# Kernel optimization log

Hardware: AMD Instinct MI355X
Metric: run time of the kernel (lower is better)

## Reference

```python
import jax, jax.numpy as jnp
import numpy as np

NUM_HEADS = 16
HEAD_DIM = 64
BSZ, SEQ, EMBED = 2, 2048, NUM_HEADS * HEAD_DIM
SCALE = HEAD_DIM ** (-0.5)
NEG = -1e9  # large negative for masked positions (finite, fp16-unsafe values avoided)


def setup_inputs() -> dict:
    key = jax.random.key(0)
    kq, kk, kv = jax.random.split(key, 3)
    q = jax.random.normal(kq, (BSZ, SEQ, EMBED), dtype=jnp.float32)
    k = jax.random.normal(kk, (BSZ, SEQ, EMBED), dtype=jnp.float32)
    v = jax.random.normal(kv, (BSZ, SEQ, EMBED), dtype=jnp.float32)
    # additive causal mask: 0 on/below diagonal, NEG above, shape (bsz,1,tgt,src)
    causal = jnp.where(jnp.tril(jnp.ones((SEQ, SEQ), dtype=bool)), 0.0, NEG).astype(jnp.float32)
    causal = jnp.broadcast_to(causal[None, None], (BSZ, 1, SEQ, SEQ))
    return {"query_states": q, "key_states": k, "value_states": v,
            "causal_attention_mask": causal}


def reference(query_states, key_states, value_states, causal_attention_mask):
    bsz, tgt_len, embed_dim = query_states.shape
    # [b, h, s, d]
    def shape_heads(t):
        return t.reshape(bsz, -1, NUM_HEADS, HEAD_DIM).transpose(0, 2, 1, 3)
    q = shape_heads(query_states * SCALE)
    k = shape_heads(key_states)
    v = shape_heads(value_states)
    # scores: [b, h, tgt, src]
    attn_weights = jnp.einsum('bhqd,bhkd->bhqk', q, k)
    attn_weights = attn_weights + causal_attention_mask  # broadcast over heads
    attn_probs = jax.nn.softmax(attn_weights, axis=-1)
    # dropout p=0.0 / eval mode -> identity
    attn_output = jnp.einsum('bhqk,bhkd->bhqd', attn_probs, v)
    attn_output = attn_output.transpose(0, 2, 1, 3).reshape(bsz, tgt_len, embed_dim)
    return attn_output
```

## Files before the change

kernel.cpp:

```cpp
#include <hip/hip_runtime.h>
#include <hip/hip_bf16.h>
#include <stdint.h>

#define BSZ 2
#define SEQ 2048
#define NHEADS 16
#define HDIM 64
#define EMBED (NHEADS * HDIM)
#define NQT 32

#define QSCALE 0.1803368801111244f
#define C2 11.5416914f

typedef unsigned short u16;
typedef unsigned int u32;
typedef __attribute__((ext_vector_type(8))) short bf16x8;
typedef __attribute__((ext_vector_type(4))) float f32x4;

#define TILE_B 8192
#define WSV_BYTE_OFF (32ull * 32 * TILE_B)

__device__ __forceinline__ u32 pkbf(float x, float y) {
  union { __hip_bfloat162 h; u32 u; } c;
  c.h = __float22bfloat162_rn(make_float2(x, y));
  return c.u;
}

__device__ __forceinline__ void gload16(const void* g, void* l) {
  __builtin_amdgcn_global_load_lds(
      (const __attribute__((address_space(1))) u32*)g,
      (__attribute__((address_space(3))) u32*)l, 16, 0, 0);
}

__global__ __launch_bounds__(256) void prep_k(const float* __restrict__ K,
                                              char* __restrict__ wsK) {
  const int t = blockIdx.x * 256 + threadIdx.x;
  const int c0 = (t & 7) * 8;
  const int h = (t >> 3) & 15;
  const size_t bs = (size_t)(t >> 7);
  const int s = (int)(bs & 2047);
  const int b = (int)(bs >> 11);
  const float* p = K + bs * EMBED + h * HDIM + c0;
  const float4 a = *reinterpret_cast<const float4*>(p);
  const float4 d = *reinterpret_cast<const float4*>(p + 4);
  uint4 out;
  out.x = pkbf(a.x, a.y); out.y = pkbf(a.z, a.w);
  out.z = pkbf(d.x, d.y); out.w = pkbf(d.z, d.w);
  const int kap = s & 63, kt = s >> 6;
  const int rho = (kap & 3) * 16 + (kap >> 2);
  char* dst = wsK + (((size_t)(b * 16 + h)) * 32 + kt) * TILE_B + rho * 128 +
              ((2 * c0) ^ ((rho & 7) << 4));
  *reinterpret_cast<uint4*>(dst) = out;
}

__global__ __launch_bounds__(256) void prep_v(const float* __restrict__ V,
                                              char* __restrict__ wsV) {
  __shared__ float tile[64][68];
  const int blk = blockIdx.x;
  const int kt = blk & 31, bh = blk >> 5;
  const int b = bh >> 4, h = bh & 15;
  const float* src = V + ((size_t)b * SEQ + kt * 64) * EMBED + h * HDIM;
  const int t = threadIdx.x;
  {
    const int row = t >> 2, c0 = (t & 3) * 16;
    const float* p = src + (size_t)row * EMBED + c0;
#pragma unroll
    for (int j = 0; j < 4; ++j)
      *reinterpret_cast<float4*>(&tile[row][c0 + 4 * j]) =
          *reinterpret_cast<const float4*>(p + 4 * j);
  }
  __syncthreads();
  const int d = t & 63, w = t >> 6;
  char* dst = wsV + ((size_t)bh * 32 + kt) * TILE_B + d * 128;
#pragma unroll
  for (int half = 0; half < 2; ++half) {
    const int kv0 = w * 8 + half * 32;
    uint4 out;
    out.x = pkbf(tile[kv0 + 0][d], tile[kv0 + 1][d]);
    out.y = pkbf(tile[kv0 + 2][d], tile[kv0 + 3][d]);
    out.z = pkbf(tile[kv0 + 4][d], tile[kv0 + 5][d]);
    out.w = pkbf(tile[kv0 + 6][d], tile[kv0 + 7][d]);
    *reinterpret_cast<uint4*>(dst + ((2 * kv0) ^ ((d & 7) << 4))) = out;
  }
}

__global__ __launch_bounds__(256, 3) void mha_fwd(const float* __restrict__ Q,
                                                  const char* __restrict__ wsK,
                                                  const char* __restrict__ wsV,
                                                  float* __restrict__ O) {
  __shared__ char Kl[2][TILE_B];
  __shared__ char Vl[2][TILE_B];
  __shared__ u16 Ps[64][72];

  const int id = ((blockIdx.x & 7) << 6) | (blockIdx.x >> 3);
  const int qlo = id & 15, bh = id >> 4;
  const int qhi = (NQT - 1) - qlo;
  const int b = bh >> 4, h = bh & 15;

  const int wave = threadIdx.x >> 6;
  const int lane = threadIdx.x & 63;
  const int fr = lane & 15;
  const int hi4 = lane >> 4;
  const int fk = hi4 * 8;
  const int crow = hi4 * 4;
  const int swz = (fr & 7) << 4;
  const int cOff0 = (hi4 * 16) ^ swz;
  const int cOff1 = cOff0 ^ 64;

  const float* qrow = Q + ((size_t)b * SEQ + wave * 16 + fr) * EMBED + h * HDIM;
  bf16x8 qlo0, qlo1, qhi0, qhi1;
  {
    union { uint4 u; bf16x8 v; } cv;
    const float* plo = qrow + (size_t)qlo * 64 * EMBED;
    const float* phi = qrow + (size_t)qhi * 64 * EMBED;
#define LOADQ(dst, base, col)                                              \
    {                                                                      \
      const float4 a = *reinterpret_cast<const float4*>((base) + (col));   \
      const float4 d = *reinterpret_cast<const float4*>((base) + (col)+4); \
      cv.u.x = pkbf(a.x * QSCALE, a.y * QSCALE);                           \
      cv.u.y = pkbf(a.z * QSCALE, a.w * QSCALE);                           \
      cv.u.z = pkbf(d.x * QSCALE, d.y * QSCALE);                           \
      cv.u.w = pkbf(d.z * QSCALE, d.w * QSCALE);                           \
      dst = cv.v;                                                          \
    }
    LOADQ(qlo0, plo, fk) LOADQ(qlo1, plo, 32 + fk)
    LOADQ(qhi0, phi, fk) LOADQ(qhi1, phi, 32 + fk)
#undef LOADQ
  }

  const char* gK = wsK + (size_t)bh * 32 * TILE_B;
  const char* gV = wsV + (size_t)bh * 32 * TILE_B;
  const int wo = wave * 2048;

  gload16(gK + wo + lane * 16, Kl[0] + wo);
  gload16(gK + wo + 1024 + lane * 16, Kl[0] + wo + 1024);
  gload16(gV + wo + lane * 16, Vl[0] + wo);
  gload16(gV + wo + 1024 + lane * 16, Vl[0] + wo + 1024);
  __syncthreads();

  const f32x4 fzero = {0.f, 0.f, 0.f, 0.f};
  f32x4 oacc_lo[4], oacc_hi[4];
  float l_lo[4], l_hi[4];
#pragma unroll
  for (int i = 0; i < 4; ++i) {
    oacc_lo[i] = fzero;
    oacc_hi[i] = fzero;
    l_lo[i] = 0.f;
    l_hi[i] = 0.f;
  }

  int cur = 0;
  for (int kt = 0; kt <= qhi; ++kt) {
    if (kt < qhi) {
      const char* nk = gK + (size_t)(kt + 1) * TILE_B;
      const char* nv = gV + (size_t)(kt + 1) * TILE_B;
      char* dK = Kl[cur ^ 1] + wo;
      char* dV = Vl[cur ^ 1] + wo;
      gload16(nk + wo + lane * 16, dK);
      gload16(nk + wo + 1024 + lane * 16, dK + 1024);
      gload16(nv + wo + lane * 16, dV);
      gload16(nv + wo + 1024 + lane * 16, dV + 1024);
    }

#pragma unroll
    for (int stream = 0; stream < 2; ++stream) {
      if (stream == 1 && kt > qlo) break;
      const bf16x8 qf0 = stream ? qlo0 : qhi0;
      const bf16x8 qf1 = stream ? qlo1 : qhi1;
      const bool diag = (kt == (stream ? qlo : qhi));
      f32x4* oacc = stream ? oacc_lo : oacc_hi;
      float* l_part = stream ? l_lo : l_hi;

      f32x4 s[4];
      __builtin_amdgcn_s_setprio(1);
#pragma unroll
      for (int n = 0; n < 4; ++n) {
        const char* krow = Kl[cur] + (n * 16 + fr) * 128;
        const bf16x8 kf0 = *reinterpret_cast<const bf16x8*>(krow + cOff0);
        const bf16x8 kf1 = *reinterpret_cast<const bf16x8*>(krow + cOff1);
        s[n] = fzero;
        s[n] = __builtin_amdgcn_mfma_f32_16x16x32_bf16(qf0, kf0, s[n], 0, 0, 0);
        s[n] = __builtin_amdgcn_mfma_f32_16x16x32_bf16(qf1, kf1, s[n], 0, 0, 0);
      }
      __builtin_amdgcn_s_setprio(0);

      if (diag) {
#pragma unroll
        for (int n = 0; n < 4; ++n)
#pragma unroll
          for (int r = 0; r < 4; ++r)
            if (4 * fr + n > wave * 16 + crow + r) s[n][r] = -1.0e30f;
      }

#pragma unroll
      for (int r = 0; r < 4; ++r) {
        const float e0 = __builtin_amdgcn_exp2f(s[0][r] - C2);
        const float e1 = __builtin_amdgcn_exp2f(s[1][r] - C2);
        const float e2 = __builtin_amdgcn_exp2f(s[2][r] - C2);
        const float e3 = __builtin_amdgcn_exp2f(s[3][r] - C2);
        l_part[r] += (e0 + e1) + (e2 + e3);
        uint2 pw;
        pw.x = pkbf(e0, e1);
        pw.y = pkbf(e2, e3);
        *reinterpret_cast<uint2*>(reinterpret_cast<char*>(&Ps[0][0]) +
                                  (wave * 16 + crow + r) * 144 + fr * 8) = pw;
      }

      __builtin_amdgcn_s_setprio(1);
#pragma unroll
      for (int kk = 0; kk < 2; ++kk) {
        const bf16x8 pf = *reinterpret_cast<const bf16x8*>(
            reinterpret_cast<const char*>(&Ps[0][0]) + (wave * 16 + fr) * 144 +
            kk * 64 + fk * 2);
#pragma unroll
        for (int nd = 0; nd < 4; ++nd) {
          const bf16x8 vf = *reinterpret_cast<const bf16x8*>(
              Vl[cur] + (nd * 16 + fr) * 128 + (kk ? cOff1 : cOff0));
          oacc[nd] = __builtin_amdgcn_mfma_f32_16x16x32_bf16(pf, vf, oacc[nd], 0, 0, 0);
        }
      }
      __builtin_amdgcn_s_setprio(0);
    }

    if (kt < qhi) __syncthreads();
    cur ^= 1;
  }

#pragma unroll
  for (int stream = 0; stream < 2; ++stream) {
    float* l_part = stream ? l_lo : l_hi;
    f32x4* oacc = stream ? oacc_lo : oacc_hi;
#pragma unroll
    for (int d = 1; d < 16; d <<= 1)
#pragma unroll
      for (int r = 0; r < 4; ++r)
        l_part[r] += __shfl_xor(l_part[r], d, 64);
    float inv_l[4];
#pragma unroll
    for (int r = 0; r < 4; ++r) inv_l[r] = 1.0f / l_part[r];
    const int qt = stream ? qlo : qhi;
    float* outg =
        O + ((size_t)b * SEQ + (size_t)qt * 64 + wave * 16) * EMBED + h * HDIM;
#pragma unroll
    for (int nd = 0; nd < 4; ++nd)
#pragma unroll
      for (int r = 0; r < 4; ++r)
        outg[(size_t)(crow + r) * EMBED + nd * 16 + fr] = oacc[nd][r] * inv_l[r];
  }
}

extern "C" void kernel_launch(void* const* d_in, const int* in_sizes, int n_in,
                              void* d_out, int out_size, void* d_ws, size_t ws_size,
                              hipStream_t stream) {
  const float* q = (const float*)d_in[0];
  const float* k = (const float*)d_in[1];
  const float* v = (const float*)d_in[2];
  float* o = (float*)d_out;
  char* wsK = (char*)d_ws;
  char* wsV = wsK + WSV_BYTE_OFF;

  prep_k<<<dim3(2048), dim3(256), 0, stream>>>(k, wsK);
  prep_v<<<dim3(1024), dim3(256), 0, stream>>>(v, wsV);
  mha_fwd<<<dim3(512), dim3(256), 0, stream>>>(q, wsK, wsV, o);
}
```

Baseline: 57.66 us.

## Split KV loop across two blocks per query pair and add combine pass

```diff
diff --git a/kernel.cpp b/kernel.cpp
--- a/kernel.cpp
+++ b/kernel.cpp
@@ -18,7 +18,10 @@
 typedef __attribute__((ext_vector_type(4))) float f32x4;
 
 #define TILE_B 8192
-#define WSV_BYTE_OFF (32ull * 32 * TILE_B)
+#define WSV_OFF (8ull * 1024 * 1024)
+#define WSO_OFF (16ull * 1024 * 1024)
+#define WSO_HALF_U16 (4ull * 1024 * 1024)
+#define WSL_OFF (32ull * 1024 * 1024)
 
 __device__ __forceinline__ u32 pkbf(float x, float y) {
   union { __hip_bfloat162 h; u32 u; } c;
@@ -26,74 +29,81 @@
   return c.u;
 }
 
+__device__ __forceinline__ u16 f2bf(float x) {
+  union { float f; u32 u; } v;
+  v.f = x;
+  u32 r = v.u + 0x7fffu + ((v.u >> 16) & 1u);
+  return (u16)(r >> 16);
+}
+
 __device__ __forceinline__ void gload16(const void* g, void* l) {
   __builtin_amdgcn_global_load_lds(
       (const __attribute__((address_space(1))) u32*)g,
       (__attribute__((address_space(3))) u32*)l, 16, 0, 0);
 }
 
-__global__ __launch_bounds__(256) void prep_k(const float* __restrict__ K,
-                                              char* __restrict__ wsK) {
-  const int t = blockIdx.x * 256 + threadIdx.x;
-  const int c0 = (t & 7) * 8;
-  const int h = (t >> 3) & 15;
-  const size_t bs = (size_t)(t >> 7);
-  const int s = (int)(bs & 2047);
-  const int b = (int)(bs >> 11);
-  const float* p = K + bs * EMBED + h * HDIM + c0;
-  const float4 a = *reinterpret_cast<const float4*>(p);
-  const float4 d = *reinterpret_cast<const float4*>(p + 4);
-  uint4 out;
-  out.x = pkbf(a.x, a.y); out.y = pkbf(a.z, a.w);
-  out.z = pkbf(d.x, d.y); out.w = pkbf(d.z, d.w);
-  const int kap = s & 63, kt = s >> 6;
-  const int rho = (kap & 3) * 16 + (kap >> 2);
-  char* dst = wsK + (((size_t)(b * 16 + h)) * 32 + kt) * TILE_B + rho * 128 +
-              ((2 * c0) ^ ((rho & 7) << 4));
-  *reinterpret_cast<uint4*>(dst) = out;
-}
-
-__global__ __launch_bounds__(256) void prep_v(const float* __restrict__ V,
-                                              char* __restrict__ wsV) {
+__global__ __launch_bounds__(256) void prep_kv(const float* __restrict__ K,
+                                               const float* __restrict__ V,
+                                               char* __restrict__ ws) {
   __shared__ float tile[64][68];
-  const int blk = blockIdx.x;
-  const int kt = blk & 31, bh = blk >> 5;
-  const int b = bh >> 4, h = bh & 15;
-  const float* src = V + ((size_t)b * SEQ + kt * 64) * EMBED + h * HDIM;
-  const int t = threadIdx.x;
-  {
-    const int row = t >> 2, c0 = (t & 3) * 16;
-    const float* p = src + (size_t)row * EMBED + c0;
-#pragma unroll
-    for (int j = 0; j < 4; ++j)
-      *reinterpret_cast<float4*>(&tile[row][c0 + 4 * j]) =
-          *reinterpret_cast<const float4*>(p + 4 * j);
-  }
-  __syncthreads();
-  const int d = t & 63, w = t >> 6;
-  char* dst = wsV + ((size_t)bh * 32 + kt) * TILE_B + d * 128;
-#pragma unroll
-  for (int half = 0; half < 2; ++half) {
-    const int kv0 = w * 8 + half * 32;
+  if (blockIdx.x < 2048) {
+    const int t = blockIdx.x * 256 + threadIdx.x;
+    const int c0 = (t & 7) * 8;
+    const int h = (t >> 3) & 15;
+    const size_t bs = (size_t)(t >> 7);
+    const int s = (int)(bs & 2047);
+    const int b = (int)(bs >> 11);
+    const float* p = K + bs * EMBED + h * HDIM + c0;
+    const float4 a = *reinterpret_cast<const float4*>(p);
+    const float4 d = *reinterpret_cast<const float4*>(p + 4);
     uint4 out;
-    out.x = pkbf(tile[kv0 + 0][d], tile[kv0 + 1][d]);
-    out.y = pkbf(tile[kv0 + 2][d], tile[kv0 + 3][d]);
-    out.z = pkbf(tile[kv0 + 4][d], tile[kv0 + 5][d]);
-    out.w = pkbf(tile[kv0 + 6][d], tile[kv0 + 7][d]);
-    *reinterpret_cast<uint4*>(dst + ((2 * kv0) ^ ((d & 7) << 4))) = out;
+    out.x = pkbf(a.x, a.y); out.y = pkbf(a.z, a.w);
+    out.z = pkbf(d.x, d.y); out.w = pkbf(d.z, d.w);
+    const int kap = s & 63, kt = s >> 6;
+    const int rho = (kap & 3) * 16 + (kap >> 2);
+    char* dst = ws + (((size_t)(b * 16 + h)) * 32 + kt) * TILE_B + rho * 128 +
+                ((2 * c0) ^ ((rho & 7) << 4));
+    *reinterpret_cast<uint4*>(dst) = out;
+  } else {
+    const int blk = blockIdx.x - 2048;
+    const int kt = blk & 31, bh = blk >> 5;
+    const int b = bh >> 4, h = bh & 15;
+    const float* src = V + ((size_t)b * SEQ + kt * 64) * EMBED + h * HDIM;
+    const int t = threadIdx.x;
+    {
+      const int row = t >> 2, c0 = (t & 3) * 16;
+      const float* p = src + (size_t)row * EMBED + c0;
+#pragma unroll
+      for (int j = 0; j < 4; ++j)
+        *reinterpret_cast<float4*>(&tile[row][c0 + 4 * j]) =
+            *reinterpret_cast<const float4*>(p + 4 * j);
+    }
+    __syncthreads();
+    const int d = t & 63, w = t >> 6;
+    char* dst = ws + WSV_OFF + ((size_t)bh * 32 + kt) * TILE_B + d * 128;
+#pragma unroll
+    for (int half = 0; half < 2; ++half) {
+      const int kv0 = w * 8 + half * 32;
+      uint4 out;
+      out.x = pkbf(tile[kv0 + 0][d], tile[kv0 + 1][d]);
+      out.y = pkbf(tile[kv0 + 2][d], tile[kv0 + 3][d]);
+      out.z = pkbf(tile[kv0 + 4][d], tile[kv0 + 5][d]);
+      out.w = pkbf(tile[kv0 + 6][d], tile[kv0 + 7][d]);
+      *reinterpret_cast<uint4*>(dst + ((2 * kv0) ^ ((d & 7) << 4))) = out;
+    }
   }
 }
 
 __global__ __launch_bounds__(256, 3) void mha_fwd(const float* __restrict__ Q,
-                                                  const char* __restrict__ wsK,
-                                                  const char* __restrict__ wsV,
-                                                  float* __restrict__ O) {
+                                                  char* __restrict__ ws) {
   __shared__ char Kl[2][TILE_B];
   __shared__ char Vl[2][TILE_B];
   __shared__ u16 Ps[64][72];
 
-  const int id = ((blockIdx.x & 7) << 6) | (blockIdx.x >> 3);
-  const int qlo = id & 15, bh = id >> 4;
+  const int id = ((blockIdx.x & 7) << 7) | (blockIdx.x >> 3);
+  const int half = id & 1;
+  const int qlo = (id >> 1) & 15;
+  const int bh = id >> 5;
   const int qhi = (NQT - 1) - qlo;
   const int b = bh >> 4, h = bh & 15;
 
@@ -128,14 +138,14 @@
 #undef LOADQ
   }
 
-  const char* gK = wsK + (size_t)bh * 32 * TILE_B;
-  const char* gV = wsV + (size_t)bh * 32 * TILE_B;
+  const char* gK = ws + (size_t)bh * 32 * TILE_B;
+  const char* gV = ws + WSV_OFF + (size_t)bh * 32 * TILE_B;
   const int wo = wave * 2048;
 
-  gload16(gK + wo + lane * 16, Kl[0] + wo);
-  gload16(gK + wo + 1024 + lane * 16, Kl[0] + wo + 1024);
-  gload16(gV + wo + lane * 16, Vl[0] + wo);
-  gload16(gV + wo + 1024 + lane * 16, Vl[0] + wo + 1024);
+  gload16(gK + (size_t)half * TILE_B + wo + lane * 16, Kl[0] + wo);
+  gload16(gK + (size_t)half * TILE_B + wo + 1024 + lane * 16, Kl[0] + wo + 1024);
+  gload16(gV + (size_t)half * TILE_B + wo + lane * 16, Vl[0] + wo);
+  gload16(gV + (size_t)half * TILE_B + wo + 1024 + lane * 16, Vl[0] + wo + 1024);
   __syncthreads();
 
   const f32x4 fzero = {0.f, 0.f, 0.f, 0.f};
@@ -150,10 +160,11 @@
   }
 
   int cur = 0;
-  for (int kt = 0; kt <= qhi; ++kt) {
-    if (kt < qhi) {
-      const char* nk = gK + (size_t)(kt + 1) * TILE_B;
-      const char* nv = gV + (size_t)(kt + 1) * TILE_B;
+  for (int kt = half; kt <= qhi; kt += 2) {
+    const bool more = (kt + 2 <= qhi);
+    if (more) {
+      const char* nk = gK + (size_t)(kt + 2) * TILE_B;
+      const char* nv = gV + (size_t)(kt + 2) * TILE_B;
       char* dK = Kl[cur ^ 1] + wo;
       char* dV = Vl[cur ^ 1] + wo;
       gload16(nk + wo + lane * 16, dK);
@@ -222,10 +233,12 @@
       __builtin_amdgcn_s_setprio(0);
     }
 
-    if (kt < qhi) __syncthreads();
+    if (more) __syncthreads();
     cur ^= 1;
   }
 
+  u16* wsO = reinterpret_cast<u16*>(ws + WSO_OFF);
+  float* wsL = reinterpret_cast<float*>(ws + WSL_OFF);
 #pragma unroll
   for (int stream = 0; stream < 2; ++stream) {
     float* l_part = stream ? l_lo : l_hi;
@@ -235,18 +248,42 @@
 #pragma unroll
       for (int r = 0; r < 4; ++r)
         l_part[r] += __shfl_xor(l_part[r], d, 64);
-    float inv_l[4];
-#pragma unroll
-    for (int r = 0; r < 4; ++r) inv_l[r] = 1.0f / l_part[r];
     const int qt = stream ? qlo : qhi;
-    float* outg =
-        O + ((size_t)b * SEQ + (size_t)qt * 64 + wave * 16) * EMBED + h * HDIM;
+    u16* Op = wsO + (size_t)half * WSO_HALF_U16 +
+              (((size_t)bh * 32 + qt) * 64) * 64;
 #pragma unroll
     for (int nd = 0; nd < 4; ++nd)
 #pragma unroll
       for (int r = 0; r < 4; ++r)
-        outg[(size_t)(crow + r) * EMBED + nd * 16 + fr] = oacc[nd][r] * inv_l[r];
-  }
+        Op[(size_t)(wave * 16 + crow + r) * 64 + nd * 16 + fr] = f2bf(oacc[nd][r]);
+    if (fr == 0) {
+      float* Lp = wsL + (size_t)half * 65536 + ((size_t)bh * 32 + qt) * 64;
+#pragma unroll
+      for (int r = 0; r < 4; ++r) Lp[wave * 16 + crow + r] = l_part[r];
+    }
+  }
+}
+
+__global__ __launch_bounds__(256) void mha_combine(const char* __restrict__ ws,
+                                                   float* __restrict__ O) {
+  const int R0 = blockIdx.x * 8 + (threadIdx.x >> 5);
+  const int dp = (threadIdx.x & 31) * 2;
+  const u16* wsO = reinterpret_cast<const u16*>(ws + WSO_OFF);
+  const float* wsL = reinterpret_cast<const float*>(ws + WSL_OFF);
+  const u32 a = *reinterpret_cast<const u32*>(wsO + (size_t)R0 * 64 + dp);
+  const u32 bb = *reinterpret_cast<const u32*>(wsO + WSO_HALF_U16 +
+                                               (size_t)R0 * 64 + dp);
+  const float inv = 1.0f / (wsL[R0] + wsL[65536 + R0]);
+  union { u32 u; float f; } c0, c1, d0, d1;
+  c0.u = (a & 0xffffu) << 16;  c1.u = a & 0xffff0000u;
+  d0.u = (bb & 0xffffu) << 16; d1.u = bb & 0xffff0000u;
+  const float o0 = (c0.f + d0.f) * inv;
+  const float o1 = (c1.f + d1.f) * inv;
+  const int bh = R0 >> 11, qt = (R0 >> 6) & 31, r = R0 & 63;
+  const int b = bh >> 4, h = bh & 15;
+  float* out = O + ((size_t)b * SEQ + qt * 64 + r) * EMBED + h * HDIM + dp;
+  out[0] = o0;
+  out[1] = o1;
 }
 
 extern "C" void kernel_launch(void* const* d_in, const int* in_sizes, int n_in,
@@ -256,10 +293,9 @@
   const float* k = (const float*)d_in[1];
   const float* v = (const float*)d_in[2];
   float* o = (float*)d_out;
-  char* wsK = (char*)d_ws;
-  char* wsV = wsK + WSV_BYTE_OFF;
-
-  prep_k<<<dim3(2048), dim3(256), 0, stream>>>(k, wsK);
-  prep_v<<<dim3(1024), dim3(256), 0, stream>>>(v, wsV);
-  mha_fwd<<<dim3(512), dim3(256), 0, stream>>>(q, wsK, wsV, o);
-}
+  char* ws = (char*)d_ws;
+
+  prep_kv<<<dim3(3072), dim3(256), 0, stream>>>(k, v, ws);
+  mha_fwd<<<dim3(1024), dim3(256), 0, stream>>>(q, ws);
+  mha_combine<<<dim3(8192), dim3(256), 0, stream>>>(ws, o);
+}
```

After: 59.93 us. 1.04x slower.

## Switch attention to 32x32 MFMA with in-register P and key-split waves

Applied to the files above, without the earlier changes.

```diff
diff --git a/kernel.cpp b/kernel.cpp
--- a/kernel.cpp
+++ b/kernel.cpp
@@ -15,10 +15,10 @@
 typedef unsigned short u16;
 typedef unsigned int u32;
 typedef __attribute__((ext_vector_type(8))) short bf16x8;
-typedef __attribute__((ext_vector_type(4))) float f32x4;
+typedef __attribute__((ext_vector_type(16))) float f32x16;
 
 #define TILE_B 8192
-#define WSV_BYTE_OFF (32ull * 32 * TILE_B)
+#define WSV_OFF (8ull * 1024 * 1024)
 
 __device__ __forceinline__ u32 pkbf(float x, float y) {
   union { __hip_bfloat162 h; u32 u; } c;
@@ -32,221 +32,249 @@
       (__attribute__((address_space(3))) u32*)l, 16, 0, 0);
 }
 
-__global__ __launch_bounds__(256) void prep_k(const float* __restrict__ K,
-                                              char* __restrict__ wsK) {
-  const int t = blockIdx.x * 256 + threadIdx.x;
-  const int c0 = (t & 7) * 8;
-  const int h = (t >> 3) & 15;
-  const size_t bs = (size_t)(t >> 7);
-  const int s = (int)(bs & 2047);
-  const int b = (int)(bs >> 11);
-  const float* p = K + bs * EMBED + h * HDIM + c0;
-  const float4 a = *reinterpret_cast<const float4*>(p);
-  const float4 d = *reinterpret_cast<const float4*>(p + 4);
-  uint4 out;
-  out.x = pkbf(a.x, a.y); out.y = pkbf(a.z, a.w);
-  out.z = pkbf(d.x, d.y); out.w = pkbf(d.z, d.w);
-  const int kap = s & 63, kt = s >> 6;
-  const int rho = (kap & 3) * 16 + (kap >> 2);
-  char* dst = wsK + (((size_t)(b * 16 + h)) * 32 + kt) * TILE_B + rho * 128 +
-              ((2 * c0) ^ ((rho & 7) << 4));
-  *reinterpret_cast<uint4*>(dst) = out;
-}
-
-__global__ __launch_bounds__(256) void prep_v(const float* __restrict__ V,
-                                              char* __restrict__ wsV) {
+__global__ __launch_bounds__(256) void prep_kv(const float* __restrict__ K,
+                                               const float* __restrict__ V,
+                                               char* __restrict__ ws) {
   __shared__ float tile[64][68];
-  const int blk = blockIdx.x;
-  const int kt = blk & 31, bh = blk >> 5;
-  const int b = bh >> 4, h = bh & 15;
-  const float* src = V + ((size_t)b * SEQ + kt * 64) * EMBED + h * HDIM;
-  const int t = threadIdx.x;
+  if (blockIdx.x < 2048) {
+    const int t = blockIdx.x * 256 + threadIdx.x;
+    const int c = t & 7;
+    const int h = (t >> 3) & 15;
+    const size_t bs = (size_t)(t >> 7);
+    const int s = (int)(bs & 2047);
+    const int b = (int)(bs >> 11);
+    const float* p = K + bs * EMBED + h * HDIM + c * 8;
+    const float4 a = *reinterpret_cast<const float4*>(p);
+    const float4 d = *reinterpret_cast<const float4*>(p + 4);
+    uint4 out;
+    out.x = pkbf(a.x, a.y); out.y = pkbf(a.z, a.w);
+    out.z = pkbf(d.x, d.y); out.w = pkbf(d.z, d.w);
+    const int kt = s >> 6, key = s & 63;
+    const int kb = key >> 5;
+    const int ks = c >> 1, hi = c & 1;
+    const int lane = hi * 32 + (key & 31);
+    char* dst = ws + ((size_t)(b * 16 + h) * 32 + kt) * TILE_B +
+                ((kb * 4 + ks) * 64 + lane) * 16;
+    *reinterpret_cast<uint4*>(dst) = out;
+  } else {
+    const int blk = blockIdx.x - 2048;
+    const int kt = blk & 31, bh = blk >> 5;
+    const int b = bh >> 4, h = bh & 15;
+    const float* src = V + ((size_t)b * SEQ + kt * 64) * EMBED + h * HDIM;
+    const int t = threadIdx.x;
+    {
+      const int row = t >> 2, c0 = (t & 3) * 16;
+      const float* p = src + (size_t)row * EMBED + c0;
+#pragma unroll
+      for (int j = 0; j < 4; ++j)
+        *reinterpret_cast<float4*>(&tile[row][c0 + 4 * j]) =
+            *reinterpret_cast<const float4*>(p + 4 * j);
+    }
+    __syncthreads();
+    const int d = t & 63;
+#pragma unroll
+    for (int halfc = 0; halfc < 2; ++halfc) {
+      const int kc = (t >> 6) + halfc * 4;
+      const int kb = kc >> 2, hi = kc & 1;
+      const int ka0 = kc * 8;
+      const int base = kb * 32 + (ka0 & 16) + hi * 4;
+      uint4 out;
+      out.x = pkbf(tile[base + 0][d], tile[base + 1][d]);
+      out.y = pkbf(tile[base + 2][d], tile[base + 3][d]);
+      out.z = pkbf(tile[base + 8][d], tile[base + 9][d]);
+      out.w = pkbf(tile[base + 10][d], tile[base + 11][d]);
+      const int lane = hi * 32 + (d & 31);
+      const int db = d >> 5;
+      const int ks2 = (kc >> 1) & 1;
+      char* dst = ws + WSV_OFF + ((size_t)bh * 32 + kt) * TILE_B +
+                  ((kb * 4 + ks2 * 2 + db) * 64 + lane) * 16;
+      *reinterpret_cast<uint4*>(dst) = out;
+    }
+  }
+}
+
+__device__ __forceinline__ void stream_step(const char* Kc, const char* Vc,
+                                            const bf16x8 q0, const bf16x8 q1,
+                                            const bf16x8 q2, const bf16x8 q3,
+                                            f32x16& o0, f32x16& o1, float& lsum,
+                                            int kb, int l, int lq, int hi,
+                                            bool diagq) {
+  f32x16 s = {};
+  __builtin_amdgcn_s_setprio(1);
   {
-    const int row = t >> 2, c0 = (t & 3) * 16;
-    const float* p = src + (size_t)row * EMBED + c0;
-#pragma unroll
-    for (int j = 0; j < 4; ++j)
-      *reinterpret_cast<float4*>(&tile[row][c0 + 4 * j]) =
-          *reinterpret_cast<const float4*>(p + 4 * j);
-  }
-  __syncthreads();
-  const int d = t & 63, w = t >> 6;
-  char* dst = wsV + ((size_t)bh * 32 + kt) * TILE_B + d * 128;
-#pragma unroll
-  for (int half = 0; half < 2; ++half) {
-    const int kv0 = w * 8 + half * 32;
-    uint4 out;
-    out.x = pkbf(tile[kv0 + 0][d], tile[kv0 + 1][d]);
-    out.y = pkbf(tile[kv0 + 2][d], tile[kv0 + 3][d]);
-    out.z = pkbf(tile[kv0 + 4][d], tile[kv0 + 5][d]);
-    out.w = pkbf(tile[kv0 + 6][d], tile[kv0 + 7][d]);
-    *reinterpret_cast<uint4*>(dst + ((2 * kv0) ^ ((d & 7) << 4))) = out;
-  }
-}
-
-__global__ __launch_bounds__(256, 3) void mha_fwd(const float* __restrict__ Q,
-                                                  const char* __restrict__ wsK,
-                                                  const char* __restrict__ wsV,
+    const bf16x8 kf0 = *reinterpret_cast<const bf16x8*>(Kc + ((kb * 4 + 0) * 64 + l) * 16);
+    s = __builtin_amdgcn_mfma_f32_32x32x16_bf16(kf0, q0, s, 0, 0, 0);
+    const bf16x8 kf1 = *reinterpret_cast<const bf16x8*>(Kc + ((kb * 4 + 1) * 64 + l) * 16);
+    s = __builtin_amdgcn_mfma_f32_32x32x16_bf16(kf1, q1, s, 0, 0, 0);
+    const bf16x8 kf2 = *reinterpret_cast<const bf16x8*>(Kc + ((kb * 4 + 2) * 64 + l) * 16);
+    s = __builtin_amdgcn_mfma_f32_32x32x16_bf16(kf2, q2, s, 0, 0, 0);
+    const bf16x8 kf3 = *reinterpret_cast<const bf16x8*>(Kc + ((kb * 4 + 3) * 64 + l) * 16);
+    s = __builtin_amdgcn_mfma_f32_32x32x16_bf16(kf3, q3, s, 0, 0, 0);
+  }
+  __builtin_amdgcn_s_setprio(0);
+
+  if (diagq) {
+#pragma unroll
+    for (int r = 0; r < 16; ++r) {
+      const int crow = (r & 3) + 8 * (r >> 2) + 4 * hi;
+      if (crow > lq) s[r] = -1.0e30f;
+    }
+  }
+
+  float e[16];
+#pragma unroll
+  for (int r = 0; r < 16; ++r) e[r] = __builtin_amdgcn_exp2f(s[r] - C2);
+  lsum += ((e[0] + e[1]) + (e[2] + e[3])) + ((e[4] + e[5]) + (e[6] + e[7])) +
+          ((e[8] + e[9]) + (e[10] + e[11])) + ((e[12] + e[13]) + (e[14] + e[15]));
+  union { u32 w[4]; bf16x8 v; } pa0, pa1;
+#pragma unroll
+  for (int i = 0; i < 4; ++i) {
+    pa0.w[i] = pkbf(e[2 * i], e[2 * i + 1]);
+    pa1.w[i] = pkbf(e[8 + 2 * i], e[8 + 2 * i + 1]);
+  }
+
+  __builtin_amdgcn_s_setprio(1);
+  {
+    const bf16x8 v00 = *reinterpret_cast<const bf16x8*>(Vc + ((kb * 4 + 0) * 64 + l) * 16);
+    o0 = __builtin_amdgcn_mfma_f32_32x32x16_bf16(pa0.v, v00, o0, 0, 0, 0);
+    const bf16x8 v01 = *reinterpret_cast<const bf16x8*>(Vc + ((kb * 4 + 1) * 64 + l) * 16);
+    o1 = __builtin_amdgcn_mfma_f32_32x32x16_bf16(pa0.v, v01, o1, 0, 0, 0);
+    const bf16x8 v10 = *reinterpret_cast<const bf16x8*>(Vc + ((kb * 4 + 2) * 64 + l) * 16);
+    o0 = __builtin_amdgcn_mfma_f32_32x32x16_bf16(pa1.v, v10, o0, 0, 0, 0);
+    const bf16x8 v11 = *reinterpret_cast<const bf16x8*>(Vc + ((kb * 4 + 3) * 64 + l) * 16);
+    o1 = __builtin_amdgcn_mfma_f32_32x32x16_bf16(pa1.v, v11, o1, 0, 0, 0);
+  }
+  __builtin_amdgcn_s_setprio(0);
+}
+
+__device__ __forceinline__ void write_stream(float* __restrict__ O, int b, int h,
+                                             int qt, int qhalf, int lq, int hi,
+                                             int l, const f32x16& o0,
+                                             const f32x16& o1,
+                                             const float* __restrict__ Obuf,
+                                             float linv) {
+  float* outg = O + ((size_t)b * SEQ + qt * 64 + qhalf * 32) * EMBED + h * HDIM;
+#pragma unroll
+  for (int r = 0; r < 16; ++r) {
+    const int crow = (r & 3) + 8 * (r >> 2) + 4 * hi;
+    const float il = __shfl(linv, crow, 64);
+    const float v0 = (o0[r] + Obuf[r * 64 + l]) * il;
+    const float v1 = (o1[r] + Obuf[1024 + r * 64 + l]) * il;
+    outg[(size_t)crow * EMBED + lq] = v0;
+    outg[(size_t)crow * EMBED + 32 + lq] = v1;
+  }
+}
+
+__global__ __launch_bounds__(256, 2) void mha_fwd(const float* __restrict__ Q,
+                                                  const char* __restrict__ ws,
                                                   float* __restrict__ O) {
-  __shared__ char Kl[2][TILE_B];
-  __shared__ char Vl[2][TILE_B];
-  __shared__ u16 Ps[64][72];
+  __shared__ __align__(16) char smem[33280];
 
   const int id = ((blockIdx.x & 7) << 6) | (blockIdx.x >> 3);
   const int qlo = id & 15, bh = id >> 4;
   const int qhi = (NQT - 1) - qlo;
   const int b = bh >> 4, h = bh & 15;
 
-  const int wave = threadIdx.x >> 6;
-  const int lane = threadIdx.x & 63;
-  const int fr = lane & 15;
-  const int hi4 = lane >> 4;
-  const int fk = hi4 * 8;
-  const int crow = hi4 * 4;
-  const int swz = (fr & 7) << 4;
-  const int cOff0 = (hi4 * 16) ^ swz;
-  const int cOff1 = cOff0 ^ 64;
-
-  const float* qrow = Q + ((size_t)b * SEQ + wave * 16 + fr) * EMBED + h * HDIM;
-  bf16x8 qlo0, qlo1, qhi0, qhi1;
+  const int wv = threadIdx.x >> 6;
+  const int l = threadIdx.x & 63;
+  const int qhalf = wv & 1, kb = wv >> 1;
+  const int lq = l & 31;
+  const int hi = l >> 5;
+
+  bf16x8 qh[4], ql[4];
   {
     union { uint4 u; bf16x8 v; } cv;
-    const float* plo = qrow + (size_t)qlo * 64 * EMBED;
-    const float* phi = qrow + (size_t)qhi * 64 * EMBED;
-#define LOADQ(dst, base, col)                                              \
-    {                                                                      \
-      const float4 a = *reinterpret_cast<const float4*>((base) + (col));   \
-      const float4 d = *reinterpret_cast<const float4*>((base) + (col)+4); \
-      cv.u.x = pkbf(a.x * QSCALE, a.y * QSCALE);                           \
-      cv.u.y = pkbf(a.z * QSCALE, a.w * QSCALE);                           \
-      cv.u.z = pkbf(d.x * QSCALE, d.y * QSCALE);                           \
-      cv.u.w = pkbf(d.z * QSCALE, d.w * QSCALE);                           \
-      dst = cv.v;                                                          \
-    }
-    LOADQ(qlo0, plo, fk) LOADQ(qlo1, plo, 32 + fk)
-    LOADQ(qhi0, phi, fk) LOADQ(qhi1, phi, 32 + fk)
-#undef LOADQ
-  }
-
-  const char* gK = wsK + (size_t)bh * 32 * TILE_B;
-  const char* gV = wsV + (size_t)bh * 32 * TILE_B;
-  const int wo = wave * 2048;
-
-  gload16(gK + wo + lane * 16, Kl[0] + wo);
-  gload16(gK + wo + 1024 + lane * 16, Kl[0] + wo + 1024);
-  gload16(gV + wo + lane * 16, Vl[0] + wo);
-  gload16(gV + wo + 1024 + lane * 16, Vl[0] + wo + 1024);
+#pragma unroll
+    for (int st = 0; st < 2; ++st) {
+      const int qt = st ? qlo : qhi;
+      const float* qp =
+          Q + ((size_t)b * SEQ + qt * 64 + qhalf * 32 + lq) * EMBED + h * HDIM + hi * 8;
+#pragma unroll
+      for (int ks = 0; ks < 4; ++ks) {
+        const float4 a = *reinterpret_cast<const float4*>(qp + ks * 16);
+        const float4 d = *reinterpret_cast<const float4*>(qp + ks * 16 + 4);
+        cv.u.x = pkbf(a.x * QSCALE, a.y * QSCALE);
+        cv.u.y = pkbf(a.z * QSCALE, a.w * QSCALE);
+        cv.u.z = pkbf(d.x * QSCALE, d.y * QSCALE);
+        cv.u.w = pkbf(d.z * QSCALE, d.w * QSCALE);
+        if (st) ql[ks] = cv.v; else qh[ks] = cv.v;
+      }
+    }
+  }
+
+  const char* gK = ws + (size_t)bh * 32 * TILE_B;
+  const char* gV = ws + WSV_OFF + (size_t)bh * 32 * TILE_B;
+
+#define STAGE(dstoff, src)                                                    \
+  {                                                                           \
+    const char* s_ = (src);                                                   \
+    gload16(s_ + wv * 2048 + l * 16, smem + (dstoff) + wv * 2048);            \
+    gload16(s_ + wv * 2048 + 1024 + l * 16, smem + (dstoff) + wv * 2048 + 1024); \
+  }
+
+  STAGE(0, gK);
+  STAGE(16384, gV);
   __syncthreads();
 
-  const f32x4 fzero = {0.f, 0.f, 0.f, 0.f};
-  f32x4 oacc_lo[4], oacc_hi[4];
-  float l_lo[4], l_hi[4];
-#pragma unroll
-  for (int i = 0; i < 4; ++i) {
-    oacc_lo[i] = fzero;
-    oacc_hi[i] = fzero;
-    l_lo[i] = 0.f;
-    l_hi[i] = 0.f;
-  }
+  f32x16 oh0 = {}, oh1 = {}, ol0 = {}, ol1 = {};
+  float lsh = 0.f, lsl = 0.f;
 
   int cur = 0;
   for (int kt = 0; kt <= qhi; ++kt) {
-    if (kt < qhi) {
-      const char* nk = gK + (size_t)(kt + 1) * TILE_B;
-      const char* nv = gV + (size_t)(kt + 1) * TILE_B;
-      char* dK = Kl[cur ^ 1] + wo;
-      char* dV = Vl[cur ^ 1] + wo;
-      gload16(nk + wo + lane * 16, dK);
-      gload16(nk + wo + 1024 + lane * 16, dK + 1024);
-      gload16(nv + wo + lane * 16, dV);
-      gload16(nv + wo + 1024 + lane * 16, dV + 1024);
-    }
-
-#pragma unroll
-    for (int stream = 0; stream < 2; ++stream) {
-      if (stream == 1 && kt > qlo) break;
-      const bf16x8 qf0 = stream ? qlo0 : qhi0;
-      const bf16x8 qf1 = stream ? qlo1 : qhi1;
-      const bool diag = (kt == (stream ? qlo : qhi));
-      f32x4* oacc = stream ? oacc_lo : oacc_hi;
-      float* l_part = stream ? l_lo : l_hi;
-
-      f32x4 s[4];
-      __builtin_amdgcn_s_setprio(1);
-#pragma unroll
-      for (int n = 0; n < 4; ++n) {
-        const char* krow = Kl[cur] + (n * 16 + fr) * 128;
-        const bf16x8 kf0 = *reinterpret_cast<const bf16x8*>(krow + cOff0);
-        const bf16x8 kf1 = *reinterpret_cast<const bf16x8*>(krow + cOff1);
-        s[n] = fzero;
-        s[n] = __builtin_amdgcn_mfma_f32_16x16x32_bf16(qf0, kf0, s[n], 0, 0, 0);
-        s[n] = __builtin_amdgcn_mfma_f32_16x16x32_bf16(qf1, kf1, s[n], 0, 0, 0);
-      }
-      __builtin_amdgcn_s_setprio(0);
-
-      if (diag) {
-#pragma unroll
-        for (int n = 0; n < 4; ++n)
-#pragma unroll
-          for (int r = 0; r < 4; ++r)
-            if (4 * fr + n > wave * 16 + crow + r) s[n][r] = -1.0e30f;
-      }
-
-#pragma unroll
-      for (int r = 0; r < 4; ++r) {
-        const float e0 = __builtin_amdgcn_exp2f(s[0][r] - C2);
-        const float e1 = __builtin_amdgcn_exp2f(s[1][r] - C2);
-        const float e2 = __builtin_amdgcn_exp2f(s[2][r] - C2);
-        const float e3 = __builtin_amdgcn_exp2f(s[3][r] - C2);
-        l_part[r] += (e0 + e1) + (e2 + e3);
-        uint2 pw;
-        pw.x = pkbf(e0, e1);
-        pw.y = pkbf(e2, e3);
-        *reinterpret_cast<uint2*>(reinterpret_cast<char*>(&Ps[0][0]) +
-                                  (wave * 16 + crow + r) * 144 + fr * 8) = pw;
-      }
-
-      __builtin_amdgcn_s_setprio(1);
-#pragma unroll
-      for (int kk = 0; kk < 2; ++kk) {
-        const bf16x8 pf = *reinterpret_cast<const bf16x8*>(
-            reinterpret_cast<const char*>(&Ps[0][0]) + (wave * 16 + fr) * 144 +
-            kk * 64 + fk * 2);
-#pragma unroll
-        for (int nd = 0; nd < 4; ++nd) {
-          const bf16x8 vf = *reinterpret_cast<const bf16x8*>(
-              Vl[cur] + (nd * 16 + fr) * 128 + (kk ? cOff1 : cOff0));
-          oacc[nd] = __builtin_amdgcn_mfma_f32_16x16x32_bf16(pf, vf, oacc[nd], 0, 0, 0);
-        }
-      }
-      __builtin_amdgcn_s_setprio(0);
-    }
-
-    if (kt < qhi) __syncthreads();
+    const bool more = kt < qhi;
+    if (more) {
+      STAGE((cur ^ 1) * 8192, gK + (size_t)(kt + 1) * TILE_B);
+      STAGE(16384 + (cur ^ 1) * 8192, gV + (size_t)(kt + 1) * TILE_B);
+    }
+    const char* Kc = smem + cur * 8192;
+    const char* Vc = smem + 16384 + cur * 8192;
+
+    {
+      const bool diag = (kt == qhi);
+      if (!(diag && kb == 1 && qhalf == 0))
+        stream_step(Kc, Vc, qh[0], qh[1], qh[2], qh[3], oh0, oh1, lsh,
+                    kb, l, lq, hi, diag && (kb == qhalf));
+    }
+    if (kt <= qlo) {
+      const bool diag = (kt == qlo);
+      if (!(diag && kb == 1 && qhalf == 0))
+        stream_step(Kc, Vc, ql[0], ql[1], ql[2], ql[3], ol0, ol1, lsl,
+                    kb, l, lq, hi, diag && (kb == qhalf));
+    }
+
+    if (more) __syncthreads();
     cur ^= 1;
   }
 
-#pragma unroll
-  for (int stream = 0; stream < 2; ++stream) {
-    float* l_part = stream ? l_lo : l_hi;
-    f32x4* oacc = stream ? oacc_lo : oacc_hi;
-#pragma unroll
-    for (int d = 1; d < 16; d <<= 1)
-#pragma unroll
-      for (int r = 0; r < 4; ++r)
-        l_part[r] += __shfl_xor(l_part[r], d, 64);
-    float inv_l[4];
-#pragma unroll
-    for (int r = 0; r < 4; ++r) inv_l[r] = 1.0f / l_part[r];
-    const int qt = stream ? qlo : qhi;
-    float* outg =
-        O + ((size_t)b * SEQ + (size_t)qt * 64 + wave * 16) * EMBED + h * HDIM;
-#pragma unroll
-    for (int nd = 0; nd < 4; ++nd)
-#pragma unroll
-      for (int r = 0; r < 4; ++r)
-        outg[(size_t)(crow + r) * EMBED + nd * 16 + fr] = oacc[nd][r] * inv_l[r];
-  }
+  __syncthreads();
+  const float l2h = lsh + __shfl_xor(lsh, 32, 64);
+  const float l2l = lsl + __shfl_xor(lsl, 32, 64);
+  float* Obuf = reinterpret_cast<float*>(smem);
+  float* Lbuf = reinterpret_cast<float*>(smem + 32768);
+
+  if (kb == 1) {
+#pragma unroll
+    for (int r = 0; r < 16; ++r) {
+      Obuf[(qhalf * 2 + 0) * 1024 + r * 64 + l] = oh0[r];
+      Obuf[(qhalf * 2 + 1) * 1024 + r * 64 + l] = oh1[r];
+      Obuf[((2 + qhalf) * 2 + 0) * 1024 + r * 64 + l] = ol0[r];
+      Obuf[((2 + qhalf) * 2 + 1) * 1024 + r * 64 + l] = ol1[r];
+    }
+    if (l < 32) {
+      Lbuf[qhalf * 32 + lq] = l2h;
+      Lbuf[(2 + qhalf) * 32 + lq] = l2l;
+    }
+  }
+  __syncthreads();
+  if (kb == 0) {
+    const float linv_h = 1.0f / (l2h + Lbuf[qhalf * 32 + lq]);
+    write_stream(O, b, h, qhi, qhalf, lq, hi, l, oh0, oh1,
+                 Obuf + (qhalf * 2) * 1024, linv_h);
+    const float linv_l = 1.0f / (l2l + Lbuf[(2 + qhalf) * 32 + lq]);
+    write_stream(O, b, h, qlo, qhalf, lq, hi, l, ol0, ol1,
+                 Obuf + ((2 + qhalf) * 2) * 1024, linv_l);
+  }
+#undef STAGE
 }
 
 extern "C" void kernel_launch(void* const* d_in, const int* in_sizes, int n_in,
@@ -256,10 +284,8 @@
   const float* k = (const float*)d_in[1];
   const float* v = (const float*)d_in[2];
   float* o = (float*)d_out;
-  char* wsK = (char*)d_ws;
-  char* wsV = wsK + WSV_BYTE_OFF;
-
-  prep_k<<<dim3(2048), dim3(256), 0, stream>>>(k, wsK);
-  prep_v<<<dim3(1024), dim3(256), 0, stream>>>(v, wsV);
-  mha_fwd<<<dim3(512), dim3(256), 0, stream>>>(q, wsK, wsV, o);
-}
+  char* ws = (char*)d_ws;
+
+  prep_kv<<<dim3(3072), dim3(256), 0, stream>>>(k, v, ws);
+  mha_fwd<<<dim3(512), dim3(256), 0, stream>>>(q, ws, o);
+}
```

Result: faster. 50.59 us (-12.3%).
